# Kernel optimization log

Measured on AMD Instinct MI355X. Metric: run time of the kernel, lower is better.

## Reference

```python
import jax, jax.numpy as jnp
import numpy as np

QMAX = 127.0  # int8 symmetric range per get_quant_min_max(torch.int8)


def setup_inputs() -> dict:
    key = jax.random.key(0)
    k1, k2, k3, k4, k5, k6 = jax.random.split(key, 6)
    B, S, IN, OUT = 4, 2048, 4096, 4096
    x = jax.random.normal(k1, (B, S, IN), dtype=jnp.float32)
    # smoothquant-style per-input-channel scale (1/scale in torch code), positive
    input_scale = jax.random.uniform(k2, (IN,), jnp.float32, 0.5, 2.0)
    # per-tensor static activation scale (positive scalar)
    act_scale = jax.random.uniform(k3, (), jnp.float32, 0.01, 0.03)
    # pre-quantized int8 weight values in [-127, 127], stored as int32
    w_int = jax.random.randint(k4, (OUT, IN), -127, 128, dtype=jnp.int32)
    # per-out-channel weight scale
    w_scale = jax.random.uniform(k5, (OUT,), jnp.float32, 0.001, 0.01)
    bias = jax.random.normal(k6, (OUT,), dtype=jnp.float32) * 0.1
    return {"x": x, "input_scale": input_scale, "act_scale": act_scale,
            "w_int": w_int, "w_scale": w_scale, "bias": bias}


def reference(x, input_scale, act_scale, w_int, w_scale, bias):
    # mode == 'quantized' path of QModule.forward with forward_module = F.linear
    # 1) smooth-scale activations, 2) static affine int8 quantize (zero_point NONE)
    xs = x * input_scale  # [B,S,IN]
    xi = jnp.clip(jnp.round(xs / act_scale), -QMAX, QMAX).astype(jnp.int32)
    # 3) integer matmul (exact, matches torch double matmul of int values + round)
    acc = jnp.einsum('bsi,oi->bso', xi, w_int)  # int32 accumulate, exact
    # 4) dequant: scale = q(q(scale_i * scale_w, f32), f32) -> plain f32 product here
    scale = act_scale * w_scale  # [OUT]
    out = acc.astype(jnp.float32) * scale + bias
    return out
```

## Files before the change

### kernel.cpp

```cpp
#include <hip/hip_runtime.h>
#include <hip/hip_bf16.h>
#include <stdint.h>

#define Mdim 8192
#define Ndim 4096
#define Kdim 4096

#define BM 256
#define BN 256
#define BK 128

typedef int v4i __attribute__((ext_vector_type(4)));

__device__ __forceinline__ void gload_lds16(const void* g, void* l) {
  __builtin_amdgcn_global_load_lds(
      (const __attribute__((address_space(1))) unsigned int*)g,
      (__attribute__((address_space(3))) unsigned int*)l,
      16 , 0 , 0 );
}

__global__ void quant_x_kernel(const float* __restrict__ x,
                               const float* __restrict__ in_scale,
                               const float* __restrict__ act_scale_p,
                               int8_t* __restrict__ xq) {
  const float inv_act = 1.0f / (*act_scale_p);
  const int64_t tid = (int64_t)blockIdx.x * blockDim.x + threadIdx.x;
  const int64_t base = tid * 16;
  const int k0 = (int)(base & (Kdim - 1));
  const float4* xv = (const float4*)(x + base);
  const float4* sv = (const float4*)(in_scale + k0);
  alignas(16) int8_t ob[16];
#pragma unroll
  for (int j = 0; j < 4; ++j) {
    float4 xx = xv[j];
    float4 ss = sv[j];
    float r0 = rintf((xx.x * ss.x) * inv_act);
    float r1 = rintf((xx.y * ss.y) * inv_act);
    float r2 = rintf((xx.z * ss.z) * inv_act);
    float r3 = rintf((xx.w * ss.w) * inv_act);
    r0 = fminf(fmaxf(r0, -127.f), 127.f);
    r1 = fminf(fmaxf(r1, -127.f), 127.f);
    r2 = fminf(fmaxf(r2, -127.f), 127.f);
    r3 = fminf(fmaxf(r3, -127.f), 127.f);
    ob[j * 4 + 0] = (int8_t)r0;
    ob[j * 4 + 1] = (int8_t)r1;
    ob[j * 4 + 2] = (int8_t)r2;
    ob[j * 4 + 3] = (int8_t)r3;
  }
  *(v4i*)(xq + base) = *(const v4i*)ob;
}

__global__ void pack_w_kernel(const int* __restrict__ w, int8_t* __restrict__ wq) {
  const int64_t tid = (int64_t)blockIdx.x * blockDim.x + threadIdx.x;
  const int64_t base = tid * 16;
  const int4* wv = (const int4*)(w + base);
  alignas(16) int8_t ob[16];
#pragma unroll
  for (int j = 0; j < 4; ++j) {
    int4 t = wv[j];
    ob[j * 4 + 0] = (int8_t)t.x;
    ob[j * 4 + 1] = (int8_t)t.y;
    ob[j * 4 + 2] = (int8_t)t.z;
    ob[j * 4 + 3] = (int8_t)t.w;
  }
  *(v4i*)(wq + base) = *(const v4i*)ob;
}

#define PBAR()                        \
  do {                                \
    asm volatile("" ::: "memory");    \
    __builtin_amdgcn_s_barrier();     \
    asm volatile("" ::: "memory");    \
  } while (0)
#define VMCNT(n) asm volatile("s_waitcnt vmcnt(" #n ")" ::: "memory")

#define MFMA16(mh)                                                        \
  do {                                                                    \
    __builtin_amdgcn_s_setprio(1);                                        \
    _Pragma("unroll") for (int i = 0; i < 4; ++i) {                       \
      _Pragma("unroll") for (int j = 0; j < 4; ++j) {                     \
        acc[(mh) * 4 + i][j] = __builtin_amdgcn_mfma_i32_16x16x64_i8(     \
            af[i], bf[j], acc[(mh) * 4 + i][j], 0, 0, 0);                 \
      }                                                                   \
    }                                                                     \
    __builtin_amdgcn_s_setprio(0);                                        \
  } while (0)

__global__ __launch_bounds__(512, 2) void gemm_i8_kernel(
    const int8_t* __restrict__ Aq, const int8_t* __restrict__ Bq,
    const float* __restrict__ w_scale, const float* __restrict__ bias,
    const float* __restrict__ act_scale_p, float* __restrict__ out) {
  __shared__ alignas(16) int8_t As[2][2][BM * 64];
  __shared__ alignas(16) int8_t Bs[2][2][BN * 64];

  const int t = threadIdx.x;

  const int lin = blockIdx.x;
  const int within = lin & 31;
  const int m_blk = (lin >> 5) * 2 + (within & 1);
  const int n_blk = within >> 1;
  const int m0 = m_blk * BM;
  const int n0 = n_blk * BN;

  const int srow = t >> 2;
  const int scol = ((t & 3) ^ ((t >> 3) & 3)) * 16;
  const int8_t* gA0 = Aq + (int64_t)(m0 + srow) * Kdim + scol;
  const int8_t* gA1 = gA0 + (int64_t)128 * Kdim;
  const int8_t* gB0 = Bq + (int64_t)(n0 + srow) * Kdim + scol;
  const int8_t* gB1 = gB0 + (int64_t)128 * Kdim;
  const int ldst = t * 16;

  const int w = t >> 6;
  const int l = t & 63;
  const int wm = (w >> 2) * 128;
  const int wn = (w & 3) * 64;
  const int lrow = l & 15;
  const int lk = ((l >> 4) ^ ((l >> 1) & 3)) * 16;
  const int abase = (wm + lrow) * 64 + lk;
  const int bbase = (wn + lrow) * 64 + lk;

  v4i acc[8][4] = {};

#define STG(MAT, buf, ks, h, koff) \
  gload_lds16(g##MAT##h + (koff) + (ks) * 64, &MAT##s[buf][ks][(h) * 8192 + ldst])

  STG(A, 0, 0, 0, 0); STG(B, 0, 0, 0, 0);
  STG(A, 0, 0, 1, 0); STG(B, 0, 0, 1, 0);
  STG(A, 0, 1, 0, 0); STG(B, 0, 1, 0, 0);
  STG(A, 0, 1, 1, 0); STG(B, 0, 1, 1, 0);
  VMCNT(4);
  PBAR();

  for (int kt = 0; kt < Kdim; kt += BK) {
    const int cur = (kt >> 7) & 1;
    const int nxt = cur ^ 1;
    int kn = kt + BK;
    if (kn >= Kdim) kn = 0;

    v4i af[4], bf[4];

#pragma unroll
    for (int j = 0; j < 4; ++j) bf[j] = *(const v4i*)&Bs[cur][0][bbase + j * 1024];
#pragma unroll
    for (int i = 0; i < 4; ++i) af[i] = *(const v4i*)&As[cur][0][abase + i * 1024];
    STG(A, nxt, 0, 0, kn); STG(B, nxt, 0, 0, kn);
    __builtin_amdgcn_s_barrier();
    MFMA16(0);
    PBAR();

#pragma unroll
    for (int i = 0; i < 4; ++i) af[i] = *(const v4i*)&As[cur][0][abase + 4096 + i * 1024];
    STG(A, nxt, 0, 1, kn); STG(B, nxt, 0, 1, kn);
    __builtin_amdgcn_s_barrier();
    MFMA16(1);
    VMCNT(4);
    PBAR();

#pragma unroll
    for (int j = 0; j < 4; ++j) bf[j] = *(const v4i*)&Bs[cur][1][bbase + j * 1024];
#pragma unroll
    for (int i = 0; i < 4; ++i) af[i] = *(const v4i*)&As[cur][1][abase + i * 1024];
    STG(A, nxt, 1, 0, kn); STG(B, nxt, 1, 0, kn);
    __builtin_amdgcn_s_barrier();
    MFMA16(0);
    PBAR();

#pragma unroll
    for (int i = 0; i < 4; ++i) af[i] = *(const v4i*)&As[cur][1][abase + 4096 + i * 1024];
    STG(A, nxt, 1, 1, kn); STG(B, nxt, 1, 1, kn);
    __builtin_amdgcn_s_barrier();
    MFMA16(1);
    VMCNT(4);
    PBAR();
  }
  VMCNT(0);

  const float act = *act_scale_p;
  const int rowbase = (l >> 4) * 4;
#pragma unroll
  for (int j = 0; j < 4; ++j) {
    const int n = n0 + wn + j * 16 + lrow;
    const float sc = act * w_scale[n];
    const float bs = bias[n];
#pragma unroll
    for (int i = 0; i < 8; ++i) {
      const int mb = m0 + wm + i * 16 + rowbase;
#pragma unroll
      for (int r = 0; r < 4; ++r) {
        out[(int64_t)(mb + r) * Ndim + n] = (float)acc[i][j][r] * sc + bs;
      }
    }
  }
}

extern "C" void kernel_launch(void* const* d_in, const int* in_sizes, int n_in,
                              void* d_out, int out_size, void* d_ws, size_t ws_size,
                              hipStream_t stream) {
  const float* x        = (const float*)d_in[0];
  const float* in_scale = (const float*)d_in[1];
  const float* actp     = (const float*)d_in[2];
  const int*   w_int    = (const int*)d_in[3];
  const float* w_scale  = (const float*)d_in[4];
  const float* bias     = (const float*)d_in[5];
  float* out = (float*)d_out;

  int8_t* Aq = (int8_t*)d_ws;
  int8_t* Bq = (int8_t*)d_ws + (size_t)Mdim * Kdim;

  {
    const int64_t nthreads = (int64_t)Mdim * Kdim / 16;
    quant_x_kernel<<<(int)(nthreads / 256), 256, 0, stream>>>(x, in_scale, actp, Aq);
  }
  {
    const int64_t nthreads = (int64_t)Ndim * Kdim / 16;
    pack_w_kernel<<<(int)(nthreads / 256), 256, 0, stream>>>(w_int, Bq);
  }
  {
    gemm_i8_kernel<<<dim3(512), 512, 0, stream>>>(Aq, Bq, w_scale, bias, actp, out);
  }
}
```

Measured before the change: 404.9 us.

## Software-pipeline LDS fragment loads one phase ahead of MFMAs with double register sets

```diff
diff --git a/kernel.cpp b/kernel.cpp
--- a/kernel.cpp
+++ b/kernel.cpp
@@ -74,13 +74,13 @@
   } while (0)
 #define VMCNT(n) asm volatile("s_waitcnt vmcnt(" #n ")" ::: "memory")
 
-#define MFMA16(mh)                                                        \
+#define MFMA16(mh, AF, BF)                                                \
   do {                                                                    \
     __builtin_amdgcn_s_setprio(1);                                        \
     _Pragma("unroll") for (int i = 0; i < 4; ++i) {                       \
       _Pragma("unroll") for (int j = 0; j < 4; ++j) {                     \
         acc[(mh) * 4 + i][j] = __builtin_amdgcn_mfma_i32_16x16x64_i8(     \
-            af[i], bf[j], acc[(mh) * 4 + i][j], 0, 0, 0);                 \
+            AF[i], BF[j], acc[(mh) * 4 + i][j], 0, 0, 0);                 \
       }                                                                   \
     }                                                                     \
     __builtin_amdgcn_s_setprio(0);                                        \
@@ -120,6 +120,7 @@
   const int bbase = (wn + lrow) * 64 + lk;
 
   v4i acc[8][4] = {};
+  v4i bf0[4], bf1[4], afA[4], afB[4];
 
 #define STG(MAT, buf, ks, h, koff) \
   gload_lds16(g##MAT##h + (koff) + (ks) * 64, &MAT##s[buf][ks][(h) * 8192 + ldst])
@@ -130,6 +131,10 @@
   STG(A, 0, 1, 1, 0); STG(B, 0, 1, 1, 0);
   VMCNT(4);
   PBAR();
+#pragma unroll
+  for (int j = 0; j < 4; ++j) bf0[j] = *(const v4i*)&Bs[0][0][bbase + j * 1024];
+#pragma unroll
+  for (int i = 0; i < 4; ++i) afA[i] = *(const v4i*)&As[0][0][abase + i * 1024];
 
   for (int kt = 0; kt < Kdim; kt += BK) {
     const int cur = (kt >> 7) & 1;
@@ -137,40 +142,38 @@
     int kn = kt + BK;
     if (kn >= Kdim) kn = 0;
 
-    v4i af[4], bf[4];
-
-#pragma unroll
-    for (int j = 0; j < 4; ++j) bf[j] = *(const v4i*)&Bs[cur][0][bbase + j * 1024];
-#pragma unroll
-    for (int i = 0; i < 4; ++i) af[i] = *(const v4i*)&As[cur][0][abase + i * 1024];
     STG(A, nxt, 0, 0, kn); STG(B, nxt, 0, 0, kn);
-    __builtin_amdgcn_s_barrier();
-    MFMA16(0);
-    PBAR();
-
-#pragma unroll
-    for (int i = 0; i < 4; ++i) af[i] = *(const v4i*)&As[cur][0][abase + 4096 + i * 1024];
+    PBAR();
+#pragma unroll
+    for (int i = 0; i < 4; ++i) afB[i] = *(const v4i*)&As[cur][0][abase + 4096 + i * 1024];
+    MFMA16(0, afA, bf0);
+    PBAR();
+
+    VMCNT(2);
     STG(A, nxt, 0, 1, kn); STG(B, nxt, 0, 1, kn);
-    __builtin_amdgcn_s_barrier();
-    MFMA16(1);
-    VMCNT(4);
-    PBAR();
-
-#pragma unroll
-    for (int j = 0; j < 4; ++j) bf[j] = *(const v4i*)&Bs[cur][1][bbase + j * 1024];
-#pragma unroll
-    for (int i = 0; i < 4; ++i) af[i] = *(const v4i*)&As[cur][1][abase + i * 1024];
+    PBAR();
+#pragma unroll
+    for (int j = 0; j < 4; ++j) bf1[j] = *(const v4i*)&Bs[cur][1][bbase + j * 1024];
+#pragma unroll
+    for (int i = 0; i < 4; ++i) afA[i] = *(const v4i*)&As[cur][1][abase + i * 1024];
+    MFMA16(1, afB, bf0);
+    PBAR();
+
     STG(A, nxt, 1, 0, kn); STG(B, nxt, 1, 0, kn);
-    __builtin_amdgcn_s_barrier();
-    MFMA16(0);
-    PBAR();
-
-#pragma unroll
-    for (int i = 0; i < 4; ++i) af[i] = *(const v4i*)&As[cur][1][abase + 4096 + i * 1024];
+    PBAR();
+#pragma unroll
+    for (int i = 0; i < 4; ++i) afB[i] = *(const v4i*)&As[cur][1][abase + 4096 + i * 1024];
+    MFMA16(0, afA, bf1);
+    PBAR();
+
+    VMCNT(2);
     STG(A, nxt, 1, 1, kn); STG(B, nxt, 1, 1, kn);
-    __builtin_amdgcn_s_barrier();
-    MFMA16(1);
-    VMCNT(4);
+    PBAR();
+#pragma unroll
+    for (int j = 0; j < 4; ++j) bf0[j] = *(const v4i*)&Bs[nxt][0][bbase + j * 1024];
+#pragma unroll
+    for (int i = 0; i < 4; ++i) afA[i] = *(const v4i*)&As[nxt][0][abase + i * 1024];
+    MFMA16(1, afB, bf1);
     PBAR();
   }
   VMCNT(0);
```

Result: slower. 425.6 us (+5.1%).

## Switch GEMM to 256x128 tiles with a three-stage K-slice LDS ring

Applied to the files above, without the earlier changes.

```diff
diff --git a/kernel.cpp b/kernel.cpp
--- a/kernel.cpp
+++ b/kernel.cpp
@@ -6,9 +6,9 @@
 #define Ndim 4096
 #define Kdim 4096
 
-#define BM 256
-#define BN 256
-#define BK 128
+#define BMt 256
+#define BNt 128
+#define NSLICE (Kdim / 64)
 
 typedef int v4i __attribute__((ext_vector_type(4)));
 
@@ -74,104 +74,100 @@
   } while (0)
 #define VMCNT(n) asm volatile("s_waitcnt vmcnt(" #n ")" ::: "memory")
 
-#define MFMA16(mh)                                                        \
+#define MFMA16(mh, AF, BF)                                                \
   do {                                                                    \
     __builtin_amdgcn_s_setprio(1);                                        \
     _Pragma("unroll") for (int i = 0; i < 4; ++i) {                       \
       _Pragma("unroll") for (int j = 0; j < 4; ++j) {                     \
         acc[(mh) * 4 + i][j] = __builtin_amdgcn_mfma_i32_16x16x64_i8(     \
-            af[i], bf[j], acc[(mh) * 4 + i][j], 0, 0, 0);                 \
+            AF[i], BF[j], acc[(mh) * 4 + i][j], 0, 0, 0);                 \
       }                                                                   \
     }                                                                     \
     __builtin_amdgcn_s_setprio(0);                                        \
   } while (0)
 
-__global__ __launch_bounds__(512, 2) void gemm_i8_kernel(
+__global__ __launch_bounds__(256, 2) void gemm_i8_kernel(
     const int8_t* __restrict__ Aq, const int8_t* __restrict__ Bq,
     const float* __restrict__ w_scale, const float* __restrict__ bias,
     const float* __restrict__ act_scale_p, float* __restrict__ out) {
-  __shared__ alignas(16) int8_t As[2][2][BM * 64];
-  __shared__ alignas(16) int8_t Bs[2][2][BN * 64];
+  __shared__ alignas(16) int8_t As[3][BMt * 64];
+  __shared__ alignas(16) int8_t Bs[3][BNt * 64];
 
   const int t = threadIdx.x;
 
   const int lin = blockIdx.x;
-  const int within = lin & 31;
-  const int m_blk = (lin >> 5) * 2 + (within & 1);
+  const int within = lin & 63;
+  const int m_blk = (lin >> 6) * 2 + (within & 1);
   const int n_blk = within >> 1;
-  const int m0 = m_blk * BM;
-  const int n0 = n_blk * BN;
+  const int m0 = m_blk * BMt;
+  const int n0 = n_blk * BNt;
 
   const int srow = t >> 2;
   const int scol = ((t & 3) ^ ((t >> 3) & 3)) * 16;
   const int8_t* gA0 = Aq + (int64_t)(m0 + srow) * Kdim + scol;
-  const int8_t* gA1 = gA0 + (int64_t)128 * Kdim;
+  const int8_t* gA1 = gA0 + (int64_t)64 * Kdim;
+  const int8_t* gA2 = gA0 + (int64_t)128 * Kdim;
+  const int8_t* gA3 = gA0 + (int64_t)192 * Kdim;
   const int8_t* gB0 = Bq + (int64_t)(n0 + srow) * Kdim + scol;
-  const int8_t* gB1 = gB0 + (int64_t)128 * Kdim;
+  const int8_t* gB1 = gB0 + (int64_t)64 * Kdim;
   const int ldst = t * 16;
 
   const int w = t >> 6;
   const int l = t & 63;
-  const int wm = (w >> 2) * 128;
-  const int wn = (w & 3) * 64;
+  const int wm = (w >> 1) * 128;
+  const int wn = (w & 1) * 64;
   const int lrow = l & 15;
   const int lk = ((l >> 4) ^ ((l >> 1) & 3)) * 16;
   const int abase = (wm + lrow) * 64 + lk;
   const int bbase = (wn + lrow) * 64 + lk;
 
   v4i acc[8][4] = {};
-
-#define STG(MAT, buf, ks, h, koff) \
-  gload_lds16(g##MAT##h + (koff) + (ks) * 64, &MAT##s[buf][ks][(h) * 8192 + ldst])
-
-  STG(A, 0, 0, 0, 0); STG(B, 0, 0, 0, 0);
-  STG(A, 0, 0, 1, 0); STG(B, 0, 0, 1, 0);
-  STG(A, 0, 1, 0, 0); STG(B, 0, 1, 0, 0);
-  STG(A, 0, 1, 1, 0); STG(B, 0, 1, 1, 0);
-  VMCNT(4);
+  v4i bf[4], afA[4], afB[4];
+
+#define STG_A012(rt, sp)                                    \
+  do {                                                      \
+    const int ko_ = (sp) * 64;                              \
+    gload_lds16(gA0 + ko_, &As[rt][ldst]);                  \
+    gload_lds16(gA1 + ko_, &As[rt][4096 + ldst]);           \
+    gload_lds16(gA2 + ko_, &As[rt][8192 + ldst]);           \
+  } while (0)
+#define STG_A3B(rt, sp)                                     \
+  do {                                                      \
+    const int ko_ = (sp) * 64;                              \
+    gload_lds16(gA3 + ko_, &As[rt][12288 + ldst]);          \
+    gload_lds16(gB0 + ko_, &Bs[rt][ldst]);                  \
+    gload_lds16(gB1 + ko_, &Bs[rt][4096 + ldst]);           \
+  } while (0)
+
+  STG_A012(0, 0); STG_A3B(0, 0);
+  STG_A012(1, 1); STG_A3B(1, 1);
+  VMCNT(6);
   PBAR();
 
-  for (int kt = 0; kt < Kdim; kt += BK) {
-    const int cur = (kt >> 7) & 1;
-    const int nxt = cur ^ 1;
-    int kn = kt + BK;
-    if (kn >= Kdim) kn = 0;
-
-    v4i af[4], bf[4];
-
-#pragma unroll
-    for (int j = 0; j < 4; ++j) bf[j] = *(const v4i*)&Bs[cur][0][bbase + j * 1024];
-#pragma unroll
-    for (int i = 0; i < 4; ++i) af[i] = *(const v4i*)&As[cur][0][abase + i * 1024];
-    STG(A, nxt, 0, 0, kn); STG(B, nxt, 0, 0, kn);
+  int ring = 0;
+  for (int s = 0; s < NSLICE; ++s) {
+    const int r = ring;
+    int rt = ring + 2; if (rt >= 3) rt -= 3;
+    int sp = s + 2; if (sp >= NSLICE) sp -= NSLICE;
+
+#pragma unroll
+    for (int j = 0; j < 4; ++j) bf[j] = *(const v4i*)&Bs[r][bbase + j * 1024];
+#pragma unroll
+    for (int i = 0; i < 4; ++i) afA[i] = *(const v4i*)&As[r][abase + i * 1024];
+    STG_A012(rt, sp);
     __builtin_amdgcn_s_barrier();
-    MFMA16(0);
+    MFMA16(0, afA, bf);
     PBAR();
 
 #pragma unroll
-    for (int i = 0; i < 4; ++i) af[i] = *(const v4i*)&As[cur][0][abase + 4096 + i * 1024];
-    STG(A, nxt, 0, 1, kn); STG(B, nxt, 0, 1, kn);
+    for (int i = 0; i < 4; ++i) afB[i] = *(const v4i*)&As[r][abase + 4096 + i * 1024];
+    STG_A3B(rt, sp);
     __builtin_amdgcn_s_barrier();
-    MFMA16(1);
-    VMCNT(4);
+    MFMA16(1, afB, bf);
+    VMCNT(6);
     PBAR();
 
-#pragma unroll
-    for (int j = 0; j < 4; ++j) bf[j] = *(const v4i*)&Bs[cur][1][bbase + j * 1024];
-#pragma unroll
-    for (int i = 0; i < 4; ++i) af[i] = *(const v4i*)&As[cur][1][abase + i * 1024];
-    STG(A, nxt, 1, 0, kn); STG(B, nxt, 1, 0, kn);
-    __builtin_amdgcn_s_barrier();
-    MFMA16(0);
-    PBAR();
-
-#pragma unroll
-    for (int i = 0; i < 4; ++i) af[i] = *(const v4i*)&As[cur][1][abase + 4096 + i * 1024];
-    STG(A, nxt, 1, 1, kn); STG(B, nxt, 1, 1, kn);
-    __builtin_amdgcn_s_barrier();
-    MFMA16(1);
-    VMCNT(4);
-    PBAR();
+    ring = ring + 1; if (ring >= 3) ring -= 3;
   }
   VMCNT(0);
 
@@ -186,8 +182,8 @@
     for (int i = 0; i < 8; ++i) {
       const int mb = m0 + wm + i * 16 + rowbase;
 #pragma unroll
-      for (int r = 0; r < 4; ++r) {
-        out[(int64_t)(mb + r) * Ndim + n] = (float)acc[i][j][r] * sc + bs;
+      for (int r2 = 0; r2 < 4; ++r2) {
+        out[(int64_t)(mb + r2) * Ndim + n] = (float)acc[i][j][r2] * sc + bs;
       }
     }
   }
@@ -216,6 +212,6 @@
     pack_w_kernel<<<(int)(nthreads / 256), 256, 0, stream>>>(w_int, Bq);
   }
   {
-    gemm_i8_kernel<<<dim3(512), 512, 0, stream>>>(Aq, Bq, w_scale, bias, actp, out);
-  }
-}
+    gemm_i8_kernel<<<dim3(1024), 256, 0, stream>>>(Aq, Bq, w_scale, bias, actp, out);
+  }
+}
```

Result: no change. 407.3 us (+0.6%).
